# Kernel tuning notes

Hardware: AMD Instinct MI355X
Metric: run time of the kernel (lower is better)

The kernel has to match this reference:

```python
import jax, jax.numpy as jnp
import numpy as np
import math

IN_FEATURES = 4096
OUT_FEATURES = 4096
P = max(IN_FEATURES, OUT_FEATURES)   # total_permutations
D = min(IN_FEATURES, OUT_FEATURES)   # diag_length
SPARSITY = 0.1
K = math.ceil(int((1.0 - SPARSITY) * IN_FEATURES * OUT_FEATURES) / D)  # 3687
ALPHA_LR = 0.01
NUM_ITER = 50


def sparse_soft_topk_mask_dykstra(alpha, k, l, num_iter):
    """Dykstra projection of alpha/l onto {0<=m<=1, sum(m)=k} (soft top-k mask)."""
    s = alpha / l
    n = s.shape[0]
    p0 = jnp.zeros_like(s)
    q0 = jnp.zeros_like(s)

    def body(carry, _):
        x, p, q = carry
        # project x+p onto hyperplane sum = k
        t = x + p
        y = t + (k - jnp.sum(t)) / n
        p = t - y
        # project y+q onto box [0, 1]
        u = y + q
        x_new = jnp.clip(u, 0.0, 1.0)
        q = u - x_new
        return (x_new, p, q), None

    (x, _, _), _ = jax.lax.scan(body, (s, p0, q0), None, length=num_iter)
    return x  # last projection is onto the box -> exact zeros / ones


def compute_weight(V, alpha):
    a = sparse_soft_topk_mask_dykstra(alpha, K, ALPHA_LR, NUM_ITER)  # (P,)
    vals = a[:, None] * V                                             # (P, D)
    i = jnp.arange(P)[:, None]
    j = jnp.arange(D)[None, :]
    if OUT_FEATURES >= IN_FEATURES:
        # pseudo-diagonal i: rows shifted by i, column j scaled by V[i, j]
        rows = (i + j) % OUT_FEATURES
        cols = jnp.broadcast_to(j, (P, D))
    else:
        # row r scaled by V[i, r], columns shifted by i
        rows = jnp.broadcast_to(j, (P, D))
        cols = (i + j) % IN_FEATURES
    W = jnp.zeros((OUT_FEATURES, IN_FEATURES), V.dtype)
    W = W.at[rows.reshape(-1), cols.reshape(-1)].add(vals.reshape(-1))
    return W


def setup_inputs() -> dict:
    key = jax.random.key(0)
    k1, k2 = jax.random.split(key)
    # kaiming_uniform_(a=sqrt(5)) over fan_in = D -> bound = sqrt(1/D)
    bound = 1.0 / np.sqrt(D)
    V = jax.random.uniform(k1, (P, D), jnp.float32, -bound, bound)
    alpha = jnp.ones((P,), jnp.float32) / IN_FEATURES
    x = jax.random.normal(k2, (512, IN_FEATURES), jnp.float32)
    return {"x": x, "V": V, "alpha": alpha}


def reference(x, V, alpha):
    W = compute_weight(V, alpha)  # (out, in)
    return x @ W.T                # F.linear(x, W)
```

## Files before the change

kernel.cpp:

```cpp
#include <hip/hip_runtime.h>
#include <hip/hip_bf16.h>
#include <stdint.h>

#define PDIM 4096
#define KSEL 3687.0f
#define NITER 50

typedef unsigned short ushort_t;
typedef __attribute__((ext_vector_type(8))) __bf16 bf16x8;
typedef __attribute__((ext_vector_type(4))) float f32x4;

typedef __attribute__((address_space(3))) void lds_void;
typedef __attribute__((address_space(1))) const void glob_void;

__device__ __forceinline__ ushort_t f32_to_bf16_rne(float f) {
  union { float f; uint32_t u; } v; v.f = f;
  uint32_t r = 0x7FFFu + ((v.u >> 16) & 1u);
  return (ushort_t)((v.u + r) >> 16);
}

__device__ __forceinline__ float bf16_to_f32(ushort_t h) {
  union { uint32_t u; float f; } v; v.u = ((uint32_t)h) << 16;
  return v.f;
}

__device__ __forceinline__ void async_cp16(const void* g, void* l) {
  __builtin_amdgcn_global_load_lds((glob_void*)g, (lds_void*)l, 16, 0, 0);
}

__global__ __launch_bounds__(256) void prep_kernel(
    const float* __restrict__ alpha, float* __restrict__ a_out,
    const float* __restrict__ x, ushort_t* __restrict__ Xb, int n4) {
  if (blockIdx.x != 0) {
    const int i = (blockIdx.x - 1) * 256 + threadIdx.x;
    if (i < n4) {
      const float4 v = ((const float4*)x)[i];
      ushort4 o;
      o.x = f32_to_bf16_rne(v.x);
      o.y = f32_to_bf16_rne(v.y);
      o.z = f32_to_bf16_rne(v.z);
      o.w = f32_to_bf16_rne(v.w);
      ((ushort4*)Xb)[i] = o;
    }
    return;
  }
  __shared__ float red[8];
  const int tid = threadIdx.x;
  const int lane = tid & 63;
  const int wv = tid >> 6;
  float xx[16], q[16];
  float p = 0.0f;
#pragma unroll
  for (int i = 0; i < 16; ++i) {
    xx[i] = alpha[i * 256 + tid] * 100.0f;
    q[i] = 0.0f;
  }
  for (int it = 0; it < NITER; ++it) {
    float t[16];
    float loc = 0.0f;
#pragma unroll
    for (int i = 0; i < 16; ++i) { t[i] = xx[i] + p; loc += t[i]; }
#pragma unroll
    for (int off = 32; off > 0; off >>= 1) loc += __shfl_down(loc, off, 64);
    const int slot = (it & 1) * 4;
    if (lane == 0) red[slot + wv] = loc;
    __syncthreads();
    const float tot = red[slot] + red[slot + 1] + red[slot + 2] + red[slot + 3];
    const float corr = (KSEL - tot) * (1.0f / 4096.0f);
    p = -corr;
#pragma unroll
    for (int i = 0; i < 16; ++i) {
      const float y = t[i] + corr;
      const float u = y + q[i];
      const float xn = fminf(fmaxf(u, 0.0f), 1.0f);
      q[i] = u - xn;
      xx[i] = xn;
    }
  }
#pragma unroll
  for (int i = 0; i < 16; ++i) a_out[i * 256 + tid] = xx[i];
}

__global__ __launch_bounds__(256) void wmat_kernel(
    const float* __restrict__ V, const float* __restrict__ a,
    ushort_t* __restrict__ Wb) {
  __shared__ float vt[192][67];
  const int t = threadIdx.x;
  const int r0 = blockIdx.x * 128;
  const int c0 = blockIdx.y * 64;
  const int dbase = (r0 - c0 - 63 + 2 * PDIM) & (PDIM - 1);
  const int csub = (t & 15) * 4;
  const int rsub = t >> 4;
#pragma unroll
  for (int i = 0; i < 12; ++i) {
    const int ld = i * 16 + rsub;
    const int d = (dbase + ld) & (PDIM - 1);
    const float av = a[d];
    const float4 vv = *(const float4*)(V + (size_t)d * PDIM + c0 + csub);
    vt[ld][csub + 0] = av * vv.x;
    vt[ld][csub + 1] = av * vv.y;
    vt[ld][csub + 2] = av * vv.z;
    vt[ld][csub + 3] = av * vv.w;
  }
  __syncthreads();
#pragma unroll
  for (int k = 0; k < 4; ++k) {
    const int ry = (t >> 3) + k * 32;
    const int cb = (t & 7) * 8;
    ushort_t pk[8];
#pragma unroll
    for (int j = 0; j < 8; ++j) {
      const int c = cb + j;
      pk[j] = f32_to_bf16_rne(vt[ry - c + 63][c]);
    }
    *(uint4*)(Wb + (size_t)(r0 + ry) * PDIM + c0 + cb) = *(const uint4*)pk;
  }
}

__global__ __launch_bounds__(256, 3) void gemm_kernel(
    const ushort_t* __restrict__ Xb, const ushort_t* __restrict__ Wb,
    ushort_t* __restrict__ par) {
  constexpr int Kdim = 4096, KQ = 1024;
  __shared__ __align__(16) ushort_t As[128 * 64];
  __shared__ __align__(16) ushort_t Bs[128 * 64];
  const int tid = threadIdx.x;
  const int lane = tid & 63;
  const int w = tid >> 6;
  const int l15 = lane & 15;
  const int quad = lane >> 4;
  const int z = blockIdx.x;
  const int nblk = blockIdx.y;
  const int mblk = blockIdx.z;
  const int m0 = mblk * 128;
  const int n0 = nblk * 128;
  const int kbase = z * KQ;
  const int arow = lane >> 3;
  const int aslot = lane & 7;

  f32x4 acc[8][2];
#pragma unroll
  for (int mt = 0; mt < 8; ++mt)
#pragma unroll
    for (int nt = 0; nt < 2; ++nt) acc[mt][nt] = (f32x4){0.f, 0.f, 0.f, 0.f};

  for (int it = 0; it < KQ / 64; ++it) {
    const int k0 = kbase + it * 64;
#pragma unroll
    for (int s = w; s < 16; s += 4) {
      const int row = s * 8 + arow;
      const int j = aslot ^ (row & 7);
      async_cp16(Xb + (size_t)(m0 + row) * Kdim + k0 + j * 8,
                 (char*)As + (size_t)s * 1024);
      async_cp16(Wb + (size_t)(n0 + row) * Kdim + k0 + j * 8,
                 (char*)Bs + (size_t)s * 1024);
    }
    __syncthreads();
#pragma unroll
    for (int kk = 0; kk < 64; kk += 32) {
      const int cj = (kk >> 3) + quad;
      bf16x8 bfv[2];
#pragma unroll
      for (int nt = 0; nt < 2; ++nt) {
        const int row = w * 32 + nt * 16 + l15;
        bfv[nt] = *(const bf16x8*)&Bs[(row * 8 + (cj ^ (row & 7))) * 8];
      }
#pragma unroll
      for (int mt = 0; mt < 8; ++mt) {
        const int row = mt * 16 + l15;
        const bf16x8 af = *(const bf16x8*)&As[(row * 8 + (cj ^ (row & 7))) * 8];
        acc[mt][0] = __builtin_amdgcn_mfma_f32_16x16x32_bf16(af, bfv[0],
                                                             acc[mt][0], 0, 0, 0);
        acc[mt][1] = __builtin_amdgcn_mfma_f32_16x16x32_bf16(af, bfv[1],
                                                             acc[mt][1], 0, 0, 0);
      }
    }
    __syncthreads();
  }
  const int tile = nblk * 4 + mblk;
  ushort_t* pbase = par + ((size_t)z * 128 + tile) * 16384;
#pragma unroll
  for (int mt = 0; mt < 8; ++mt) {
#pragma unroll
    for (int nt = 0; nt < 2; ++nt) {
      const int slot = mt * 2 + nt;
      ushort4 o;
      o.x = f32_to_bf16_rne(acc[mt][nt][0]);
      o.y = f32_to_bf16_rne(acc[mt][nt][1]);
      o.z = f32_to_bf16_rne(acc[mt][nt][2]);
      o.w = f32_to_bf16_rne(acc[mt][nt][3]);
      *(ushort4*)(pbase + (size_t)(slot * 256 + tid) * 4) = o;
    }
  }
}

__global__ __launch_bounds__(256) void combine_kernel(
    const ushort_t* __restrict__ par, float* __restrict__ out) {
  const int tile = blockIdx.x >> 2;
  const int qh = blockIdx.x & 3;
  const int nblk = tile >> 2;
  const int mblk = tile & 3;
  const int m0 = mblk * 128;
  const int n0 = nblk * 128;
  const int tid = threadIdx.x;
  const int lane = tid & 63;
  const int w = tid >> 6;
  const int l15 = lane & 15;
  const int quad = lane >> 4;
#pragma unroll
  for (int ss = 0; ss < 4; ++ss) {
    const int slot = qh * 4 + ss;
    float s0 = 0.f, s1 = 0.f, s2 = 0.f, s3 = 0.f;
#pragma unroll
    for (int z = 0; z < 4; ++z) {
      const ushort4 v = *(const ushort4*)(par +
          ((size_t)z * 128 + tile) * 16384 + (size_t)(slot * 256 + tid) * 4);
      s0 += bf16_to_f32(v.x);
      s1 += bf16_to_f32(v.y);
      s2 += bf16_to_f32(v.z);
      s3 += bf16_to_f32(v.w);
    }
    const int mt = slot >> 1;
    const int nt = slot & 1;
    const int mb = m0 + mt * 16 + quad * 4;
    const int n = n0 + w * 32 + nt * 16 + l15;
    out[(size_t)(mb + 0) * PDIM + n] = s0;
    out[(size_t)(mb + 1) * PDIM + n] = s1;
    out[(size_t)(mb + 2) * PDIM + n] = s2;
    out[(size_t)(mb + 3) * PDIM + n] = s3;
  }
}

extern "C" void kernel_launch(void* const* d_in, const int* in_sizes, int n_in,
                              void* d_out, int out_size, void* d_ws,
                              size_t ws_size, hipStream_t stream) {
  const float* x = (const float*)d_in[0];
  const float* V = (const float*)d_in[1];
  const float* alpha = (const float*)d_in[2];
  float* out = (float*)d_out;
  const int M = in_sizes[0] / PDIM;

  float* a_mask = (float*)d_ws;
  ushort_t* Xb = (ushort_t*)((char*)d_ws + 16 * 1024);
  ushort_t* Wb = Xb + (size_t)M * PDIM;
  ushort_t* par = Wb + (size_t)PDIM * PDIM;

  const int n4x = (M * PDIM) / 4;
  prep_kernel<<<1 + (n4x + 255) / 256, 256, 0, stream>>>(alpha, a_mask, x, Xb,
                                                         n4x);
  wmat_kernel<<<dim3(PDIM / 128, PDIM / 64), 256, 0, stream>>>(V, a_mask, Wb);
  gemm_kernel<<<dim3(4, PDIM / 128, M / 128), 256, 0, stream>>>(Xb, Wb, par);
  combine_kernel<<<512, 256, 0, stream>>>(par, out);
}
```

Baseline: 157.1 us.

## Prefetch V into cache during Dykstra prep and use DPP wave reduction

Adds 2048 blocks to the prep kernel that load all of V (64 MB) and discard the values, so that V sits in the cache hierarchy while block 0 runs the serial Dykstra iterations. wmat_kernel can then read V from cache rather than HBM. The wave sum in the Dykstra loop now uses DPP row operations instead of shuffle-down, with the result read from lane 63. This relies on 64 MB fitting in the MI355X last-level cache and not being evicted by the x conversion. The extra blocks also add HBM traffic to a kernel that was previously short.

```diff
diff --git a/kernel.cpp b/kernel.cpp
--- a/kernel.cpp
+++ b/kernel.cpp
@@ -28,11 +28,40 @@
   __builtin_amdgcn_global_load_lds((glob_void*)g, (lds_void*)l, 16, 0, 0);
 }
 
+__device__ __forceinline__ float wave_sum_dpp(float x) {
+  float s = x;
+  int t;
+  t = __builtin_amdgcn_update_dpp(0, __float_as_int(s), 0x111, 0xF, 0xF, true);
+  s += __int_as_float(t);
+  t = __builtin_amdgcn_update_dpp(0, __float_as_int(s), 0x112, 0xF, 0xF, true);
+  s += __int_as_float(t);
+  t = __builtin_amdgcn_update_dpp(0, __float_as_int(s), 0x114, 0xF, 0xF, true);
+  s += __int_as_float(t);
+  t = __builtin_amdgcn_update_dpp(0, __float_as_int(s), 0x118, 0xF, 0xF, true);
+  s += __int_as_float(t);
+  t = __builtin_amdgcn_update_dpp(0, __float_as_int(s), 0x142, 0xA, 0xF, true);
+  s += __int_as_float(t);
+  t = __builtin_amdgcn_update_dpp(0, __float_as_int(s), 0x143, 0xC, 0xF, true);
+  s += __int_as_float(t);
+  return s;
+}
+
 __global__ __launch_bounds__(256) void prep_kernel(
     const float* __restrict__ alpha, float* __restrict__ a_out,
-    const float* __restrict__ x, ushort_t* __restrict__ Xb, int n4) {
+    const float* __restrict__ x, ushort_t* __restrict__ Xb, int n4,
+    const float* __restrict__ V) {
+  if (blockIdx.x >= 1 && blockIdx.x <= 2048) {
+    const float4* V4 = (const float4*)V;
+    const int base = (blockIdx.x - 1) * 2048 + (int)threadIdx.x;
+#pragma unroll
+    for (int i = 0; i < 8; ++i) {
+      const float4 vv = V4[base + i * 256];
+      asm volatile("" :: "v"(vv.x), "v"(vv.y), "v"(vv.z), "v"(vv.w));
+    }
+    return;
+  }
   if (blockIdx.x != 0) {
-    const int i = (blockIdx.x - 1) * 256 + threadIdx.x;
+    const int i = (blockIdx.x - 2049) * 256 + threadIdx.x;
     if (i < n4) {
       const float4 v = ((const float4*)x)[i];
       ushort4 o;
@@ -60,10 +89,9 @@
     float loc = 0.0f;
 #pragma unroll
     for (int i = 0; i < 16; ++i) { t[i] = xx[i] + p; loc += t[i]; }
-#pragma unroll
-    for (int off = 32; off > 0; off >>= 1) loc += __shfl_down(loc, off, 64);
+    loc = wave_sum_dpp(loc);
     const int slot = (it & 1) * 4;
-    if (lane == 0) red[slot + wv] = loc;
+    if (lane == 63) red[slot + wv] = loc;
     __syncthreads();
     const float tot = red[slot] + red[slot + 1] + red[slot + 2] + red[slot + 3];
     const float corr = (KSEL - tot) * (1.0f / 4096.0f);
@@ -245,8 +273,8 @@
   ushort_t* par = Wb + (size_t)PDIM * PDIM;
 
   const int n4x = (M * PDIM) / 4;
-  prep_kernel<<<1 + (n4x + 255) / 256, 256, 0, stream>>>(alpha, a_mask, x, Xb,
-                                                         n4x);
+  prep_kernel<<<1 + 2048 + (n4x + 255) / 256, 256, 0, stream>>>(
+      alpha, a_mask, x, Xb, n4x, V);
   wmat_kernel<<<dim3(PDIM / 128, PDIM / 64), 256, 0, stream>>>(V, a_mask, Wb);
   gemm_kernel<<<dim3(4, PDIM / 128, M / 128), 256, 0, stream>>>(Xb, Wb, par);
   combine_kernel<<<512, 256, 0, stream>>>(par, out);
```

Result: faster. 148.8 us (median of 2 runs) (-5.3%).
